# Kernel tuning notes

Hardware: AMD Instinct MI355X
Metric: run time of the kernel (lower is better)

Reference implementation:

```python
import jax, jax.numpy as jnp
import numpy as np

NUM_SEGMENTS = 256


def setup_inputs() -> dict:
    key = jax.random.key(0)
    k1, k2 = jax.random.split(key)
    n, d = 1048576, 128
    inp = jax.random.normal(k1, (n, d), dtype=jnp.float32)
    batch_seg = jnp.sort(jax.random.randint(k2, (n,), 0, NUM_SEGMENTS, dtype=jnp.int32))
    return {"inp": inp, "batch_seg": batch_seg}


def reference(inp, batch_seg):
    # Segment mean: equivalent to the TF while_loop that, for each unique id,
    # gathers its rows and takes the mean. With sorted ids covering 0..B-1,
    # output row i corresponds to segment id i (order of first appearance).
    sums = jax.ops.segment_sum(inp, batch_seg, num_segments=NUM_SEGMENTS)  # (B, d)
    counts = jax.ops.segment_sum(jnp.ones((inp.shape[0],), inp.dtype), batch_seg,
                                 num_segments=NUM_SEGMENTS)  # (B,)
    counts = jnp.maximum(counts, 1)  # guard (all segments present by construction)
    return sums / counts[:, None]
```

## Files before the change

### kernel.cpp

```cpp
#include <hip/hip_runtime.h>

#define NSEG 256
#define D 128
#define COL4 (D / 4)

__global__ void init_starts_kernel(int* starts, int n) {
    int i = blockIdx.x * blockDim.x + threadIdx.x;
    if (i <= NSEG) starts[i] = n;
}

__global__ void find_starts_kernel(const int* __restrict__ seg, int n, int* __restrict__ starts) {
    int i = blockIdx.x * blockDim.x + threadIdx.x;
    if (i < n) {
        int s = seg[i];
        if (i == 0 || seg[i - 1] != s) starts[s] = i;
    }
}

__global__ __launch_bounds__(1024) void seg_mean_kernel(const float4* __restrict__ inp,
                                                        const int* __restrict__ starts,
                                                        float* __restrict__ out, int n) {
    const int s = blockIdx.x;
    __shared__ int sh_bounds[2];
    if (threadIdx.x == 0) {
        int st = starts[s];
        int en = n;
        for (int t = s + 1; t <= NSEG; ++t) {
            int v = starts[t];
            if (v < n) { en = v; break; }
        }
        sh_bounds[0] = st;
        sh_bounds[1] = en;
    }
    __syncthreads();
    const int start = sh_bounds[0];
    const int end   = sh_bounds[1];

    const int col  = threadIdx.x & (COL4 - 1);
    const int slot = threadIdx.x >> 5;

    float4 acc = make_float4(0.f, 0.f, 0.f, 0.f);
    #pragma unroll 4
    for (int r = start + slot; r < end; r += 32) {
        float4 v = inp[(size_t)r * COL4 + col];
        acc.x += v.x; acc.y += v.y; acc.z += v.z; acc.w += v.w;
    }

    __shared__ float4 red[32][COL4];
    red[slot][col] = acc;
    __syncthreads();
    #pragma unroll
    for (int stride = 16; stride >= 1; stride >>= 1) {
        if (slot < stride) {
            float4 a = red[slot][col];
            float4 b = red[slot + stride][col];
            a.x += b.x; a.y += b.y; a.z += b.z; a.w += b.w;
            red[slot][col] = a;
        }
        __syncthreads();
    }

    if (slot == 0) {
        int cnt = end - start;
        float inv = 1.0f / (float)(cnt > 1 ? cnt : 1);
        float4 a = red[0][col];
        float4 o = make_float4(a.x * inv, a.y * inv, a.z * inv, a.w * inv);
        ((float4*)out)[(size_t)s * COL4 + col] = o;
    }
}

extern "C" void kernel_launch(void* const* d_in, const int* in_sizes, int n_in,
                              void* d_out, int out_size, void* d_ws, size_t ws_size,
                              hipStream_t stream) {
    const float* inp = (const float*)d_in[0];
    const int* seg   = (const int*)d_in[1];
    float* out       = (float*)d_out;
    const int n = in_sizes[1];

    int* starts = (int*)d_ws;

    init_starts_kernel<<<2, 256, 0, stream>>>(starts, n);
    find_starts_kernel<<<(n + 255) / 256, 256, 0, stream>>>(seg, n, starts);
    seg_mean_kernel<<<NSEG, 1024, 0, stream>>>((const float4*)inp, starts, out, n);
}
```

Before: 673.8 us.

## Split each segment across multiple blocks with a separate finalize reduction

Each segment's row range is now split into 16 chunks, each handled by a 256-thread block that writes a partial sum to workspace. A new finalize kernel adds the partials and divides by the count. The old grid of only 256 blocks of 1024 threads underfilled the GPU for a 512 MB streaming read, and the split is meant to raise parallelism and memory-level concurrency. The cost is an extra kernel launch and a small round trip through workspace.

```diff
diff --git a/kernel.cpp b/kernel.cpp
--- a/kernel.cpp
+++ b/kernel.cpp
@@ -3,6 +3,8 @@
 #define NSEG 256
 #define D 128
 #define COL4 (D / 4)
+#define SPLIT 16
+
 
 __global__ void init_starts_kernel(int* starts, int n) {
     int i = blockIdx.x * blockDim.x + threadIdx.x;
@@ -17,10 +19,12 @@
     }
 }
 
-__global__ __launch_bounds__(1024) void seg_mean_kernel(const float4* __restrict__ inp,
-                                                        const int* __restrict__ starts,
-                                                        float* __restrict__ out, int n) {
-    const int s = blockIdx.x;
+__global__ __launch_bounds__(256) void seg_partial_kernel(const float4* __restrict__ inp,
+                                                          const int* __restrict__ starts,
+                                                          float4* __restrict__ psums, int n) {
+    const int s = blockIdx.x >> 4;
+    const int k = blockIdx.x & (SPLIT - 1);
+
     __shared__ int sh_bounds[2];
     if (threadIdx.x == 0) {
         int st = starts[s];
@@ -36,21 +40,28 @@
     const int start = sh_bounds[0];
     const int end   = sh_bounds[1];
 
+    int len = end - start;
+    if (len < 0) len = 0;
+    const int chunk = (len + SPLIT - 1) / SPLIT;
+    int r0 = start + k * chunk;
+    int r1 = r0 + chunk;
+    if (r1 > end) r1 = end;
+
     const int col  = threadIdx.x & (COL4 - 1);
     const int slot = threadIdx.x >> 5;
 
     float4 acc = make_float4(0.f, 0.f, 0.f, 0.f);
     #pragma unroll 4
-    for (int r = start + slot; r < end; r += 32) {
+    for (int r = r0 + slot; r < r1; r += 8) {
         float4 v = inp[(size_t)r * COL4 + col];
         acc.x += v.x; acc.y += v.y; acc.z += v.z; acc.w += v.w;
     }
 
-    __shared__ float4 red[32][COL4];
+    __shared__ float4 red[8][COL4];
     red[slot][col] = acc;
     __syncthreads();
     #pragma unroll
-    for (int stride = 16; stride >= 1; stride >>= 1) {
+    for (int stride = 4; stride >= 1; stride >>= 1) {
         if (slot < stride) {
             float4 a = red[slot][col];
             float4 b = red[slot + stride][col];
@@ -61,12 +72,32 @@
     }
 
     if (slot == 0) {
-        int cnt = end - start;
-        float inv = 1.0f / (float)(cnt > 1 ? cnt : 1);
-        float4 a = red[0][col];
-        float4 o = make_float4(a.x * inv, a.y * inv, a.z * inv, a.w * inv);
-        ((float4*)out)[(size_t)s * COL4 + col] = o;
+        psums[((size_t)k * NSEG + s) * COL4 + col] = red[0][col];
     }
+}
+
+__global__ __launch_bounds__(64) void finalize_kernel(const float4* __restrict__ psums,
+                                                      const int* __restrict__ starts,
+                                                      float4* __restrict__ out, int n) {
+    const int s   = blockIdx.x * 2 + (threadIdx.x >> 5);
+    const int col = threadIdx.x & 31;
+
+    int start = starts[s];
+    int end = n;
+    for (int t = s + 1; t <= NSEG; ++t) {
+        int v = starts[t];
+        if (v < n) { end = v; break; }
+    }
+    int cnt = end - start;
+    float inv = 1.0f / (float)(cnt > 1 ? cnt : 1);
+
+    float4 a = make_float4(0.f, 0.f, 0.f, 0.f);
+    #pragma unroll
+    for (int k = 0; k < SPLIT; ++k) {
+        float4 v = psums[((size_t)k * NSEG + s) * COL4 + col];
+        a.x += v.x; a.y += v.y; a.z += v.z; a.w += v.w;
+    }
+    out[(size_t)s * COL4 + col] = make_float4(a.x * inv, a.y * inv, a.z * inv, a.w * inv);
 }
 
 extern "C" void kernel_launch(void* const* d_in, const int* in_sizes, int n_in,
@@ -77,9 +108,11 @@
     float* out       = (float*)d_out;
     const int n = in_sizes[1];
 
-    int* starts = (int*)d_ws;
+    int* starts    = (int*)d_ws;
+    float4* psums  = (float4*)((char*)d_ws + 4096);
 
     init_starts_kernel<<<2, 256, 0, stream>>>(starts, n);
     find_starts_kernel<<<(n + 255) / 256, 256, 0, stream>>>(seg, n, starts);
-    seg_mean_kernel<<<NSEG, 1024, 0, stream>>>((const float4*)inp, starts, out, n);
+    seg_partial_kernel<<<NSEG * SPLIT, 256, 0, stream>>>((const float4*)inp, starts, psums, n);
+    finalize_kernel<<<NSEG / 2, 64, 0, stream>>>(psums, starts, (float4*)out, n);
 }
```

Result: no change. 679.8 us (+0.9%).

## Split segment mean into row chunks with atomic accumulation and finalize pass

Applied to the files above, without the earlier changes.

Replaces the one-block-per-segment reduction (256 blocks) with a chunked scheme: 2048 blocks each process 512-row chunks, reduce in shared memory and atomically add partial sums and counts into a workspace, then a finalize kernel divides by counts. This spreads the 512MB streaming read across all CUs instead of only 256 blocks, and drops the separate segment-start search. Loads use nontemporal hints. The cost is float atomics (nondeterministic summation order) and extra zero and finalize launches.

```diff
diff --git a/kernel.cpp b/kernel.cpp
--- a/kernel.cpp
+++ b/kernel.cpp
@@ -3,70 +3,108 @@
 #define NSEG 256
 #define D 128
 #define COL4 (D / 4)
+#define ROWS_PER_CHUNK 512
+#define MAIN_BLOCKS 2048
 
-__global__ void init_starts_kernel(int* starts, int n) {
-    int i = blockIdx.x * blockDim.x + threadIdx.x;
-    if (i <= NSEG) starts[i] = n;
+typedef float f32x4 __attribute__((ext_vector_type(4)));
+
+
+__global__ __launch_bounds__(256) void zero_ws(float* __restrict__ sums, int* __restrict__ cnt) {
+    int i = blockIdx.x * 256 + threadIdx.x;
+    if (i < NSEG * D) sums[i] = 0.f;
+    if (i < NSEG) cnt[i] = 0;
 }
 
-__global__ void find_starts_kernel(const int* __restrict__ seg, int n, int* __restrict__ starts) {
-    int i = blockIdx.x * blockDim.x + threadIdx.x;
-    if (i < n) {
-        int s = seg[i];
-        if (i == 0 || seg[i - 1] != s) starts[s] = i;
+__global__ __launch_bounds__(256) void seg_sum_kernel(const f32x4* __restrict__ inp,
+                                                      const int* __restrict__ seg,
+                                                      float* __restrict__ sums,
+                                                      int* __restrict__ cnt, int n) {
+    __shared__ int  sh_seg[ROWS_PER_CHUNK];
+    __shared__ f32x4 red[8][COL4];
+
+    const int tid  = threadIdx.x;
+    const int col  = tid & (COL4 - 1);
+    const int slot = tid >> 5;
+    const int nchunks = (n + ROWS_PER_CHUNK - 1) / ROWS_PER_CHUNK;
+
+    for (int c = blockIdx.x; c < nchunks; c += gridDim.x) {
+        const int base = c * ROWS_PER_CHUNK;
+        const int rows = min(ROWS_PER_CHUNK, n - base);
+
+        if (rows == ROWS_PER_CHUNK) {
+            ((int2*)sh_seg)[tid] = ((const int2*)(seg + base))[tid];
+        } else {
+            for (int j = tid; j < rows; j += 256) sh_seg[j] = seg[base + j];
+        }
+        __syncthreads();
+
+        const bool uniform = (sh_seg[0] == sh_seg[rows - 1]);
+
+        if (uniform) {
+            const int sid = sh_seg[0];
+            f32x4 acc = {0.f, 0.f, 0.f, 0.f};
+            #pragma unroll 4
+            for (int r = slot; r < rows; r += 8) {
+                f32x4 v = __builtin_nontemporal_load(&inp[(size_t)(base + r) * COL4 + col]);
+                acc += v;
+            }
+            red[slot][col] = acc;
+            __syncthreads();
+            #pragma unroll
+            for (int st = 4; st >= 1; st >>= 1) {
+                if (slot < st) red[slot][col] += red[slot + st][col];
+                __syncthreads();
+            }
+            if (slot == 0) {
+                f32x4 a = red[0][col];
+                atomicAdd(&sums[sid * D + col * 4 + 0], a[0]);
+                atomicAdd(&sums[sid * D + col * 4 + 1], a[1]);
+                atomicAdd(&sums[sid * D + col * 4 + 2], a[2]);
+                atomicAdd(&sums[sid * D + col * 4 + 3], a[3]);
+                if (col == 0) atomicAdd(&cnt[sid], rows);
+            }
+            __syncthreads();
+        } else {
+            f32x4 acc = {0.f, 0.f, 0.f, 0.f};
+            int cur = -1, runcnt = 0;
+            for (int r = slot; r < rows; r += 8) {
+                int sid = sh_seg[r];
+                if (sid != cur) {
+                    if (runcnt) {
+                        atomicAdd(&sums[cur * D + col * 4 + 0], acc[0]);
+                        atomicAdd(&sums[cur * D + col * 4 + 1], acc[1]);
+                        atomicAdd(&sums[cur * D + col * 4 + 2], acc[2]);
+                        atomicAdd(&sums[cur * D + col * 4 + 3], acc[3]);
+                        if (col == 0) atomicAdd(&cnt[cur], runcnt);
+                    }
+                    cur = sid;
+                    acc = (f32x4){0.f, 0.f, 0.f, 0.f};
+                    runcnt = 0;
+                }
+                f32x4 v = __builtin_nontemporal_load(&inp[(size_t)(base + r) * COL4 + col]);
+                acc += v;
+                runcnt++;
+            }
+            if (runcnt) {
+                atomicAdd(&sums[cur * D + col * 4 + 0], acc[0]);
+                atomicAdd(&sums[cur * D + col * 4 + 1], acc[1]);
+                atomicAdd(&sums[cur * D + col * 4 + 2], acc[2]);
+                atomicAdd(&sums[cur * D + col * 4 + 3], acc[3]);
+                if (col == 0) atomicAdd(&cnt[cur], runcnt);
+            }
+            __syncthreads();
+        }
     }
 }
 
-__global__ __launch_bounds__(1024) void seg_mean_kernel(const float4* __restrict__ inp,
-                                                        const int* __restrict__ starts,
-                                                        float* __restrict__ out, int n) {
-    const int s = blockIdx.x;
-    __shared__ int sh_bounds[2];
-    if (threadIdx.x == 0) {
-        int st = starts[s];
-        int en = n;
-        for (int t = s + 1; t <= NSEG; ++t) {
-            int v = starts[t];
-            if (v < n) { en = v; break; }
-        }
-        sh_bounds[0] = st;
-        sh_bounds[1] = en;
-    }
-    __syncthreads();
-    const int start = sh_bounds[0];
-    const int end   = sh_bounds[1];
-
-    const int col  = threadIdx.x & (COL4 - 1);
-    const int slot = threadIdx.x >> 5;
-
-    float4 acc = make_float4(0.f, 0.f, 0.f, 0.f);
-    #pragma unroll 4
-    for (int r = start + slot; r < end; r += 32) {
-        float4 v = inp[(size_t)r * COL4 + col];
-        acc.x += v.x; acc.y += v.y; acc.z += v.z; acc.w += v.w;
-    }
-
-    __shared__ float4 red[32][COL4];
-    red[slot][col] = acc;
-    __syncthreads();
-    #pragma unroll
-    for (int stride = 16; stride >= 1; stride >>= 1) {
-        if (slot < stride) {
-            float4 a = red[slot][col];
-            float4 b = red[slot + stride][col];
-            a.x += b.x; a.y += b.y; a.z += b.z; a.w += b.w;
-            red[slot][col] = a;
-        }
-        __syncthreads();
-    }
-
-    if (slot == 0) {
-        int cnt = end - start;
-        float inv = 1.0f / (float)(cnt > 1 ? cnt : 1);
-        float4 a = red[0][col];
-        float4 o = make_float4(a.x * inv, a.y * inv, a.z * inv, a.w * inv);
-        ((float4*)out)[(size_t)s * COL4 + col] = o;
-    }
+__global__ __launch_bounds__(256) void finalize_kernel(const float* __restrict__ sums,
+                                                       const int* __restrict__ cnt,
+                                                       float* __restrict__ out) {
+    int i = blockIdx.x * 256 + threadIdx.x;
+    int s = i >> 7;
+    int c = cnt[s];
+    float inv = 1.0f / (float)(c > 1 ? c : 1);
+    out[i] = sums[i] * inv;
 }
 
 extern "C" void kernel_launch(void* const* d_in, const int* in_sizes, int n_in,
@@ -77,9 +115,14 @@
     float* out       = (float*)d_out;
     const int n = in_sizes[1];
 
-    int* starts = (int*)d_ws;
+    float* sums = (float*)d_ws;
+    int* cnt    = (int*)((char*)d_ws + NSEG * D * 4);
 
-    init_starts_kernel<<<2, 256, 0, stream>>>(starts, n);
-    find_starts_kernel<<<(n + 255) / 256, 256, 0, stream>>>(seg, n, starts);
-    seg_mean_kernel<<<NSEG, 1024, 0, stream>>>((const float4*)inp, starts, out, n);
+    zero_ws<<<(NSEG * D + 255) / 256, 256, 0, stream>>>(sums, cnt);
+
+    int nchunks = (n + ROWS_PER_CHUNK - 1) / ROWS_PER_CHUNK;
+    int grid = nchunks < MAIN_BLOCKS ? nchunks : MAIN_BLOCKS;
+    seg_sum_kernel<<<grid, 256, 0, stream>>>((const f32x4*)inp, seg, sums, cnt, n);
+
+    finalize_kernel<<<(NSEG * D + 255) / 256, 256, 0, stream>>>(sums, cnt, out);
 }
```

After: 658.4 us. 2.3% less time.
